# Optimization experiments

Hardware: AMD Instinct MI355X
Metric: run time of the kernel (lower is better)

The kernel has to match this reference:

```python
import jax, jax.numpy as jnp
import numpy as np

B, IN_SHAPE, EXP_SHAPE, HID, NB_CLASSES = 64, 10000, 53, 1500, 2048


def setup_inputs() -> dict:
    key = jax.random.key(0)
    ks = jax.random.split(key, 8)
    gos = jax.random.uniform(ks[0], (B, IN_SHAPE), dtype=jnp.float32)
    exp_x = jax.random.uniform(ks[1], (B, EXP_SHAPE), dtype=jnp.float32)
    # FlatModel params (torch Linear: y = x @ W.T + b; store pre-transposed)
    W1 = jax.random.normal(ks[2], (IN_SHAPE, HID), dtype=jnp.float32) * (1.0 / np.sqrt(IN_SHAPE))
    b1 = jnp.zeros((HID,), dtype=jnp.float32)
    W2 = jax.random.normal(ks[3], (HID + EXP_SHAPE, NB_CLASSES), dtype=jnp.float32) * (1.0 / np.sqrt(HID + EXP_SHAPE))
    b2 = jnp.zeros((NB_CLASSES,), dtype=jnp.float32)
    # HPO adjacency (non-trainable buffer in the original; values in [0,1))
    hpo_matrix = jax.random.uniform(ks[4], (NB_CLASSES, NB_CLASSES), dtype=jnp.float32)
    return {"gos": gos, "exp_x": exp_x, "W1": W1, "b1": b1, "W2": W2, "b2": b2, "hpo_matrix": hpo_matrix}


def reference(gos, exp_x, W1, b1, W2, b2, hpo_matrix):
    # FlatModel (eval mode: dropout is identity). torch F.gelu default = exact erf gelu.
    h = jax.nn.gelu(gos @ W1 + b1, approximate=False)          # (B, HID)
    x = jnp.concatenate([h, exp_x], axis=1)                     # (B, HID+EXP)
    flat = jax.nn.sigmoid(x @ W2 + b2)                          # (B, C)
    # HPOLayer + permute + MaxPool1d(C): out[b,j] = max_i flat[b,j] * M[i,j]
    out = jnp.max(flat[:, None, :] * hpo_matrix[None, :, :], axis=1)  # (B, C)
    return out
```

## Files before the change

### kernel.cpp

```cpp
#include <hip/hip_runtime.h>
#include <math.h>

#define B64 64
#define IN_SH 10000
#define GOSLD 10240
#define EXP_SH 53
#define HID 1500
#define NPAD1 1536
#define NBC 2048
#define K2 1553
#define XLD 1664
#define KS1 20
#define KCH1 512
#define KST1 16
#define KS2 13
#define KCH2 128
#define KST2 4

using short8  = __attribute__((ext_vector_type(8))) short;
using floatx4 = __attribute__((ext_vector_type(4))) float;
using uintx4  = __attribute__((ext_vector_type(4))) unsigned int;

__device__ __forceinline__ unsigned short f2bf(float f) {
    unsigned u = __float_as_uint(f);
    u += 0x7fffu + ((u >> 16) & 1u);
    return (unsigned short)(u >> 16);
}

__global__ __launch_bounds__(256) void cvt_gos(const float* __restrict__ g,
                                               unsigned short* __restrict__ gb) {
    int idx = blockIdx.x * 256 + threadIdx.x;
    int b = idx / (GOSLD / 8);
    int k = (idx % (GOSLD / 8)) * 8;
    unsigned int o[4] = {0u, 0u, 0u, 0u};
    if (k < IN_SH) {
        const float* p = g + (size_t)b * IN_SH + k;
        #pragma unroll
        for (int i = 0; i < 4; i++) {
            float lo = p[2 * i], hi = p[2 * i + 1];
            o[i] = (unsigned)f2bf(lo) | ((unsigned)f2bf(hi) << 16);
        }
    }
    uintx4 v; v.x = o[0]; v.y = o[1]; v.z = o[2]; v.w = o[3];
    *(uintx4*)(gb + (size_t)b * GOSLD + k) = v;
}

__global__ __launch_bounds__(256) void colmax(const float* __restrict__ M,
                                              unsigned int* __restrict__ cmf) {
    int j  = blockIdx.x * 256 + threadIdx.x;
    int i0 = blockIdx.y * 64;
    float m = 0.0f;
    #pragma unroll 16
    for (int i = i0; i < i0 + 64; i++)
        m = fmaxf(m, M[(size_t)i * NBC + j]);
    atomicMax(cmf + j, __float_as_uint(m));
}

__global__ __launch_bounds__(256) void mfma_gemm(
    const float* __restrict__ W, const unsigned short* __restrict__ Bm,
    float* __restrict__ part, int N, int Npad, int K, int ldw, int ldb,
    int kchunk, int ksteps)
{
    int tid  = threadIdx.x;
    int w    = tid >> 6;
    int lane = tid & 63;
    int q    = lane >> 4;
    int l15  = lane & 15;
    int n0   = blockIdx.x * 64;
    int k0   = blockIdx.y * kchunk;
    int cW   = n0 + 16 * w + l15;
    bool nok = cW < N;

    floatx4 acc[4];
    #pragma unroll
    for (int s = 0; s < 4; s++) acc[s] = (floatx4){0.f, 0.f, 0.f, 0.f};

    const unsigned short* brow0 = Bm + (size_t)l15 * ldb;

    float  wv[8];
    uintx4 bv[4];
    {
        int kb = k0 + q * 8;
        #pragma unroll
        for (int j = 0; j < 8; j++) {
            int k = kb + j;
            wv[j] = (nok && k < K) ? W[(size_t)k * ldw + cW] : 0.f;
        }
        #pragma unroll
        for (int s = 0; s < 4; s++)
            bv[s] = *(const uintx4*)(brow0 + (size_t)s * 16 * ldb + kb);
    }

    for (int st = 0; st < ksteps; st++) {
        int stn = (st + 1 < ksteps) ? st + 1 : st;
        int kb  = k0 + stn * 32 + q * 8;
        float  wn[8];
        uintx4 bn[4];
        #pragma unroll
        for (int j = 0; j < 8; j++) {
            int k = kb + j;
            wn[j] = (nok && k < K) ? W[(size_t)k * ldw + cW] : 0.f;
        }
        #pragma unroll
        for (int s = 0; s < 4; s++)
            bn[s] = *(const uintx4*)(brow0 + (size_t)s * 16 * ldb + kb);

        short8 af;
        #pragma unroll
        for (int j = 0; j < 8; j++) af[j] = (short)f2bf(wv[j]);
        #pragma unroll
        for (int s = 0; s < 4; s++) {
            short8 bf8 = __builtin_bit_cast(short8, bv[s]);
            acc[s] = __builtin_amdgcn_mfma_f32_16x16x32_bf16(af, bf8, acc[s], 0, 0, 0);
        }

        #pragma unroll
        for (int j = 0; j < 8; j++) wv[j] = wn[j];
        #pragma unroll
        for (int s = 0; s < 4; s++) bv[s] = bn[s];
    }

    size_t base = (size_t)blockIdx.y * Npad * 64;
    int nrow = n0 + 16 * w + q * 4;
    #pragma unroll
    for (int s = 0; s < 4; s++) {
        #pragma unroll
        for (int r = 0; r < 4; r++)
            part[base + (size_t)(nrow + r) * 64 + s * 16 + l15] = acc[s][r];
    }
}

__global__ __launch_bounds__(256) void combine1(
    const float* __restrict__ part, const float* __restrict__ b1,
    const float* __restrict__ expx, unsigned short* __restrict__ X)
{
    int idx = blockIdx.x * 256 + threadIdx.x;
    int b = idx & 63;
    int n = idx >> 6;
    float v = 0.f;
    if (n < HID) {
        float s = 0.f;
        #pragma unroll
        for (int c = 0; c < KS1; c++)
            s += part[((size_t)c * NPAD1 + n) * 64 + b];
        s += b1[n];
        v = 0.5f * s * (1.0f + erff(s * 0.70710678118654752f));
    } else if (n < HID + EXP_SH) {
        v = expx[b * EXP_SH + (n - HID)];
    }
    X[(size_t)b * XLD + n] = f2bf(v);
}

__global__ __launch_bounds__(256) void final_k(
    const float* __restrict__ part2, const float* __restrict__ b2,
    const unsigned int* __restrict__ cmf, float* __restrict__ out)
{
    int idx = blockIdx.x * 256 + threadIdx.x;
    int b = idx & 63;
    int j = idx >> 6;
    float s = 0.f;
    #pragma unroll
    for (int c = 0; c < KS2; c++)
        s += part2[((size_t)c * NBC + j) * 64 + b];
    s += b2[j];
    float sig = 1.0f / (1.0f + expf(-s));
    out[(size_t)b * NBC + j] = sig * __uint_as_float(cmf[j]);
}

extern "C" void kernel_launch(void* const* d_in, const int* in_sizes, int n_in,
                              void* d_out, int out_size, void* d_ws, size_t ws_size,
                              hipStream_t stream) {
    const float* gos  = (const float*)d_in[0];
    const float* expx = (const float*)d_in[1];
    const float* W1   = (const float*)d_in[2];
    const float* b1   = (const float*)d_in[3];
    const float* W2   = (const float*)d_in[4];
    const float* b2   = (const float*)d_in[5];
    const float* hpo  = (const float*)d_in[6];
    float* out = (float*)d_out;

    char* ws = (char*)d_ws;
    unsigned short* gosB = (unsigned short*)ws;
    float* part1 = (float*)(ws + 1310720);
    unsigned short* X = (unsigned short*)(ws + 1310720 + 7864320);
    float* part2 = (float*)(ws + 1310720 + 7864320 + 212992);
    unsigned int* cmf = (unsigned int*)(ws + 1310720 + 7864320 + 212992 + 6815744);

    hipMemsetAsync(cmf, 0, NBC * sizeof(unsigned int), stream);

    cvt_gos<<<(B64 * (GOSLD / 8)) / 256, 256, 0, stream>>>(gos, gosB);
    colmax<<<dim3(NBC / 256, 32), 256, 0, stream>>>(hpo, cmf);

    mfma_gemm<<<dim3(NPAD1 / 64, KS1), 256, 0, stream>>>(
        W1, gosB, part1, HID, NPAD1, IN_SH, HID, GOSLD, KCH1, KST1);

    combine1<<<(B64 * XLD) / 256, 256, 0, stream>>>(part1, b1, expx, X);

    mfma_gemm<<<dim3(NBC / 64, KS2), 256, 0, stream>>>(
        W2, X, part2, NBC, NBC, K2, NBC, XLD, KCH2, KST2);

    final_k<<<(B64 * NBC) / 256, 256, 0, stream>>>(part2, b2, cmf, out);
}
```

Baseline: 170.5 us.

## Fuse preprocessing kernels, deepen GEMM prefetch, double first-GEMM split-K

Merges the bf16 conversion and the column-max kernels into one launch. The column max now writes per-chunk partial maxima, which final_k reduces, so the memset and atomics go away. The GEMM loads two k-steps ahead instead of one and gains a launch_bounds occupancy hint. The first GEMM's split-K goes from 20 to 40 chunks for more blocks, at the cost of twice the partial-sum traffic in combine1, which still sums only KS1 chunks through the macro.

```diff
diff --git a/kernel.cpp b/kernel.cpp
--- a/kernel.cpp
+++ b/kernel.cpp
@@ -10,12 +10,13 @@
 #define NBC 2048
 #define K2 1553
 #define XLD 1664
-#define KS1 20
-#define KCH1 512
-#define KST1 16
+#define KS1 40
+#define KCH1 256
+#define KST1 8
 #define KS2 13
 #define KCH2 128
 #define KST2 4
+#define CMCH 32
 
 using short8  = __attribute__((ext_vector_type(8))) short;
 using floatx4 = __attribute__((ext_vector_type(4))) float;
@@ -27,36 +28,54 @@
     return (unsigned short)(u >> 16);
 }
 
-__global__ __launch_bounds__(256) void cvt_gos(const float* __restrict__ g,
-                                               unsigned short* __restrict__ gb) {
-    int idx = blockIdx.x * 256 + threadIdx.x;
-    int b = idx / (GOSLD / 8);
-    int k = (idx % (GOSLD / 8)) * 8;
-    unsigned int o[4] = {0u, 0u, 0u, 0u};
-    if (k < IN_SH) {
-        const float* p = g + (size_t)b * IN_SH + k;
-        #pragma unroll
-        for (int i = 0; i < 4; i++) {
-            float lo = p[2 * i], hi = p[2 * i + 1];
-            o[i] = (unsigned)f2bf(lo) | ((unsigned)f2bf(hi) << 16);
+__global__ __launch_bounds__(256) void pre_k(const float* __restrict__ g,
+                                             unsigned short* __restrict__ gb,
+                                             const float* __restrict__ M,
+                                             float* __restrict__ cm) {
+    int bi = blockIdx.x;
+    if (bi < 320) {
+        int idx = bi * 256 + threadIdx.x;
+        int b = idx / (GOSLD / 8);
+        int k = (idx % (GOSLD / 8)) * 8;
+        unsigned int o[4] = {0u, 0u, 0u, 0u};
+        if (k < IN_SH) {
+            const float* p = g + (size_t)b * IN_SH + k;
+            #pragma unroll
+            for (int i = 0; i < 4; i++) {
+                float lo = p[2 * i], hi = p[2 * i + 1];
+                o[i] = (unsigned)f2bf(lo) | ((unsigned)f2bf(hi) << 16);
+            }
         }
-    }
-    uintx4 v; v.x = o[0]; v.y = o[1]; v.z = o[2]; v.w = o[3];
-    *(uintx4*)(gb + (size_t)b * GOSLD + k) = v;
-}
-
-__global__ __launch_bounds__(256) void colmax(const float* __restrict__ M,
-                                              unsigned int* __restrict__ cmf) {
-    int j  = blockIdx.x * 256 + threadIdx.x;
-    int i0 = blockIdx.y * 64;
-    float m = 0.0f;
-    #pragma unroll 16
-    for (int i = i0; i < i0 + 64; i++)
-        m = fmaxf(m, M[(size_t)i * NBC + j]);
-    atomicMax(cmf + j, __float_as_uint(m));
-}
-
-__global__ __launch_bounds__(256) void mfma_gemm(
+        uintx4 v; v.x = o[0]; v.y = o[1]; v.z = o[2]; v.w = o[3];
+        *(uintx4*)(gb + (size_t)b * GOSLD + k) = v;
+    } else {
+        int ci = bi - 320;
+        int j  = (ci & 7) * 256 + threadIdx.x;
+        int i0 = (ci >> 3) * 64;
+        float m = 0.0f;
+        #pragma unroll 16
+        for (int i = i0; i < i0 + 64; i++)
+            m = fmaxf(m, M[(size_t)i * NBC + j]);
+        cm[(ci >> 3) * NBC + j] = m;
+    }
+}
+
+__device__ __forceinline__ void load_step(
+    const float* __restrict__ W, const unsigned short* __restrict__ brow0,
+    int kb, int K, int ldw, int ldb, int cW, bool nok,
+    float wv[8], uintx4 bv[4])
+{
+    #pragma unroll
+    for (int j = 0; j < 8; j++) {
+        int k = kb + j;
+        wv[j] = (nok && k < K) ? W[(size_t)k * ldw + cW] : 0.f;
+    }
+    #pragma unroll
+    for (int s = 0; s < 4; s++)
+        bv[s] = *(const uintx4*)(brow0 + (size_t)s * 16 * ldb + kb);
+}
+
+__global__ __launch_bounds__(256, 4) void mfma_gemm(
     const float* __restrict__ W, const unsigned short* __restrict__ Bm,
     float* __restrict__ part, int N, int Npad, int K, int ldw, int ldb,
     int kchunk, int ksteps)
@@ -70,6 +89,7 @@
     int k0   = blockIdx.y * kchunk;
     int cW   = n0 + 16 * w + l15;
     bool nok = cW < N;
+    int qk   = q * 8;
 
     floatx4 acc[4];
     #pragma unroll
@@ -77,47 +97,34 @@
 
     const unsigned short* brow0 = Bm + (size_t)l15 * ldb;
 
-    float  wv[8];
-    uintx4 bv[4];
+    float  wv[2][8];
+    uintx4 bv[2][4];
+    load_step(W, brow0, k0 + qk, K, ldw, ldb, cW, nok, wv[0], bv[0]);
     {
-        int kb = k0 + q * 8;
-        #pragma unroll
-        for (int j = 0; j < 8; j++) {
-            int k = kb + j;
-            wv[j] = (nok && k < K) ? W[(size_t)k * ldw + cW] : 0.f;
-        }
-        #pragma unroll
-        for (int s = 0; s < 4; s++)
-            bv[s] = *(const uintx4*)(brow0 + (size_t)s * 16 * ldb + kb);
+        int s1 = (ksteps > 1) ? 1 : 0;
+        load_step(W, brow0, k0 + s1 * 32 + qk, K, ldw, ldb, cW, nok, wv[1], bv[1]);
     }
 
     for (int st = 0; st < ksteps; st++) {
-        int stn = (st + 1 < ksteps) ? st + 1 : st;
-        int kb  = k0 + stn * 32 + q * 8;
-        float  wn[8];
-        uintx4 bn[4];
-        #pragma unroll
-        for (int j = 0; j < 8; j++) {
-            int k = kb + j;
-            wn[j] = (nok && k < K) ? W[(size_t)k * ldw + cW] : 0.f;
-        }
-        #pragma unroll
-        for (int s = 0; s < 4; s++)
-            bn[s] = *(const uintx4*)(brow0 + (size_t)s * 16 * ldb + kb);
+        int p   = st & 1;
+        int stn = (st + 2 < ksteps) ? st + 2 : ksteps - 1;
+        float  wt[8];
+        uintx4 bt[4];
+        load_step(W, brow0, k0 + stn * 32 + qk, K, ldw, ldb, cW, nok, wt, bt);
 
         short8 af;
         #pragma unroll
-        for (int j = 0; j < 8; j++) af[j] = (short)f2bf(wv[j]);
+        for (int j = 0; j < 8; j++) af[j] = (short)f2bf(wv[p][j]);
         #pragma unroll
         for (int s = 0; s < 4; s++) {
-            short8 bf8 = __builtin_bit_cast(short8, bv[s]);
+            short8 bf8 = __builtin_bit_cast(short8, bv[p][s]);
             acc[s] = __builtin_amdgcn_mfma_f32_16x16x32_bf16(af, bf8, acc[s], 0, 0, 0);
         }
 
         #pragma unroll
-        for (int j = 0; j < 8; j++) wv[j] = wn[j];
-        #pragma unroll
-        for (int s = 0; s < 4; s++) bv[s] = bn[s];
+        for (int j = 0; j < 8; j++) wv[p][j] = wt[j];
+        #pragma unroll
+        for (int s = 0; s < 4; s++) bv[p][s] = bt[s];
     }
 
     size_t base = (size_t)blockIdx.y * Npad * 64;
@@ -153,7 +160,7 @@
 
 __global__ __launch_bounds__(256) void final_k(
     const float* __restrict__ part2, const float* __restrict__ b2,
-    const unsigned int* __restrict__ cmf, float* __restrict__ out)
+    const float* __restrict__ cm, float* __restrict__ out)
 {
     int idx = blockIdx.x * 256 + threadIdx.x;
     int b = idx & 63;
@@ -164,7 +171,10 @@
         s += part2[((size_t)c * NBC + j) * 64 + b];
     s += b2[j];
     float sig = 1.0f / (1.0f + expf(-s));
-    out[(size_t)b * NBC + j] = sig * __uint_as_float(cmf[j]);
+    float m = 0.f;
+    #pragma unroll
+    for (int c = 0; c < CMCH; c++) m = fmaxf(m, cm[c * NBC + j]);
+    out[(size_t)b * NBC + j] = sig * m;
 }
 
 extern "C" void kernel_launch(void* const* d_in, const int* in_sizes, int n_in,
@@ -182,14 +192,11 @@
     char* ws = (char*)d_ws;
     unsigned short* gosB = (unsigned short*)ws;
     float* part1 = (float*)(ws + 1310720);
-    unsigned short* X = (unsigned short*)(ws + 1310720 + 7864320);
-    float* part2 = (float*)(ws + 1310720 + 7864320 + 212992);
-    unsigned int* cmf = (unsigned int*)(ws + 1310720 + 7864320 + 212992 + 6815744);
-
-    hipMemsetAsync(cmf, 0, NBC * sizeof(unsigned int), stream);
-
-    cvt_gos<<<(B64 * (GOSLD / 8)) / 256, 256, 0, stream>>>(gos, gosB);
-    colmax<<<dim3(NBC / 256, 32), 256, 0, stream>>>(hpo, cmf);
+    unsigned short* X = (unsigned short*)(ws + 1310720 + 15728640);
+    float* part2 = (float*)(ws + 1310720 + 15728640 + 212992);
+    float* cm    = (float*)(ws + 1310720 + 15728640 + 212992 + 6815744);
+
+    pre_k<<<576, 256, 0, stream>>>(gos, gosB, hpo, cm);
 
     mfma_gemm<<<dim3(NPAD1 / 64, KS1), 256, 0, stream>>>(
         W1, gosB, part1, HID, NPAD1, IN_SH, HID, GOSLD, KCH1, KST1);
@@ -199,5 +206,5 @@
     mfma_gemm<<<dim3(NBC / 64, KS2), 256, 0, stream>>>(
         W2, X, part2, NBC, NBC, K2, NBC, XLD, KCH2, KST2);
 
-    final_k<<<(B64 * NBC) / 256, 256, 0, stream>>>(part2, b2, cmf, out);
-}
+    final_k<<<(B64 * NBC) / 256, 256, 0, stream>>>(part2, b2, cm, out);
+}
```

New measurement: 250.6 us. +47.0%, slower.
